# Kernel optimization log

Measured on AMD Instinct MI355X. Metric: run time of the kernel, lower is better.

The kernel has to match this reference:

```python
import jax, jax.numpy as jnp
import numpy as np

N, E = 50000, 800000
D = 64          # output_dim == d_s == d_e
H = 128         # psi hidden width
PSI_IN = 2 * D + 2 * D + D  # 320


def setup_inputs() -> dict:
    key = jax.random.key(0)
    ks = jax.random.split(key, 12)
    scale = lambda fan_in: 1.0 / np.sqrt(fan_in)
    return {
        "h_d_prev": jax.random.normal(ks[0], (N, D), jnp.float32),
        "h_s": jax.random.normal(ks[1], (N, D), jnp.float32),
        "edge_feat": jax.random.normal(ks[2], (E, D), jnp.float32),
        "sender": jax.random.randint(ks[3], (E,), 0, N, jnp.int32),
        "receiver": jax.random.randint(ks[4], (E,), 0, N, jnp.int32),
        # psi MLP params (all layers use relu, incl. last: final_activation=None)
        "W0": jax.random.normal(ks[5], (PSI_IN, H), jnp.float32) * scale(PSI_IN),
        "b0": jnp.zeros((H,), jnp.float32),
        "W1": jax.random.normal(ks[6], (H, H), jnp.float32) * scale(H),
        "b1": jnp.zeros((H,), jnp.float32),
        "W2": jax.random.normal(ks[7], (H, D), jnp.float32) * scale(H),
        "b2": jnp.zeros((D,), jnp.float32),
        # final linear transform W (no bias)
        "Wm": jax.random.normal(ks[8], (D, D), jnp.float32) * scale(D),
    }


def reference(h_d_prev, h_s, edge_feat, sender, receiver, W0, b0, W1, b1, W2, b2, Wm):
    # gather node feats to edges
    h_di = h_d_prev[sender]      # [E, D]
    h_dj = h_d_prev[receiver]    # [E, D]
    h_si = h_s[sender]           # [E, D]
    h_sj = h_s[receiver]         # [E, D]
    psi_in = jnp.concatenate([h_si, h_sj, h_di, h_dj, edge_feat], axis=-1)  # [E, 320]
    # psi MLP: relu on every layer (final_activation=None keeps default relu)
    x = jax.nn.relu(psi_in @ W0 + b0)
    x = jax.nn.relu(x @ W1 + b1)
    psi = jax.nn.relu(x @ W2 + b2)          # [E, D]
    s_ij = psi * (h_dj - h_di)              # [E, D]
    agg = jax.ops.segment_sum(s_ij, receiver, num_segments=h_d_prev.shape[0])  # [N, D]
    return h_d_prev + agg @ Wm
```

## Files before the change

### kernel.cpp

```cpp
#include <hip/hip_runtime.h>

#define NN   50000
#define EE   800000
#define DD   64
#define HH   128
#define KIN  320
#define TILE_E 128

typedef __bf16 bf16x8 __attribute__((ext_vector_type(8)));
typedef float  f32x4  __attribute__((ext_vector_type(4)));

#if __has_builtin(__builtin_amdgcn_cvt_pk_bf16_f32)
typedef __bf16 bf16x2_t __attribute__((ext_vector_type(2)));
__device__ __forceinline__ unsigned int pk2(float a, float b) {
  union { bf16x2_t v; unsigned int u; } cv;
  cv.v = __builtin_amdgcn_cvt_pk_bf16_f32(a, b);
  return cv.u;
}
__device__ __forceinline__ unsigned short f2bf(float a) {
  return (unsigned short)(pk2(a, a) & 0xFFFFu);
}
#else
__device__ __forceinline__ unsigned short f2bf(float f) {
  union { float f; unsigned int u; } v; v.f = f;
  unsigned int u = v.u + 0x7FFFu + ((v.u >> 16) & 1u);
  return (unsigned short)(u >> 16);
}
__device__ __forceinline__ unsigned int pk2(float a, float b) {
  return (unsigned int)f2bf(a) | ((unsigned int)f2bf(b) << 16);
}
#endif

__device__ __forceinline__ float bf2f(unsigned short b) {
  union { unsigned int u; float f; } v; v.u = ((unsigned int)b) << 16; return v.f;
}

__device__ __forceinline__ int psiIdx(int row, int kk) {
  return ((((row >> 4) * 10 + (kk >> 5)) << 6) + ((row & 15) << 2) + ((kk >> 3) & 3)) * 8
         + (kk & 7);
}

__global__ __launch_bounds__(256) void prep_all(
    const float* __restrict__ hd, const float* __restrict__ hs,
    const float* __restrict__ W0, const float* __restrict__ W1,
    const float* __restrict__ W2,
    unsigned short* __restrict__ hdb, unsigned short* __restrict__ hsb,
    unsigned short* __restrict__ WT0, unsigned short* __restrict__ WT1,
    unsigned short* __restrict__ WT2, float* __restrict__ agg) {
  int b = blockIdx.x;
  int t = b * 256 + threadIdx.x;
  if (b < 3125) {
    *(float4*)(agg + (size_t)t * 4) = (float4){0.f, 0.f, 0.f, 0.f};
    const int n = NN * DD / 8;
    const float* src; unsigned short* dst; int i;
    if (t < n) { src = hd; dst = hdb; i = t; }
    else       { src = hs; dst = hsb; i = t - n; }
    float4 a = *(const float4*)(src + (size_t)i * 8);
    float4 c = *(const float4*)(src + (size_t)i * 8 + 4);
    uint4 w;
    w.x = pk2(a.x, a.y); w.y = pk2(a.z, a.w);
    w.z = pk2(c.x, c.y); w.w = pk2(c.z, c.w);
    *(uint4*)(dst + (size_t)i * 8) = w;
  } else {
    int u = t - 3125 * 256;
    if (u < KIN * HH) {
      int k = u / HH, n2 = u % HH;
      WT0[n2 * KIN + k] = f2bf(W0[u]);
    } else if (u < KIN * HH + HH * HH) {
      int v = u - KIN * HH; int k = v / HH, n2 = v % HH;
      WT1[n2 * HH + k] = f2bf(W1[v]);
    } else {
      int v = u - KIN * HH - HH * HH; int k = v / DD, n2 = v % DD;
      WT2[n2 * HH + k] = f2bf(W2[v]);
    }
  }
}

__global__ __launch_bounds__(512, 4) void edge_mlp(
    const unsigned short* __restrict__ hdb,
    const unsigned short* __restrict__ hsb,
    const float* __restrict__ ef,
    const int* __restrict__ snd,
    const int* __restrict__ rcv,
    const unsigned short* __restrict__ WT0,
    const float* __restrict__ b0,
    const unsigned short* __restrict__ WT1,
    const float* __restrict__ b1,
    const unsigned short* __restrict__ WT2,
    const float* __restrict__ b2,
    float* __restrict__ agg)
{
  __shared__ __align__(16) unsigned short psi[TILE_E * KIN];

  const int tid  = threadIdx.x;
  const int e0   = blockIdx.x * TILE_E;
  const int wv   = tid >> 6;
  const int lane = tid & 63;
  const int ln   = lane & 15;
  const int quad = lane >> 4;
  const int mtb  = (wv >> 2) * 4;

  int ridx[16];
  #pragma unroll
  for (int mt = 0; mt < 4; ++mt)
    #pragma unroll
    for (int i = 0; i < 4; ++i)
      ridx[mt * 4 + i] = rcv[e0 + (mtb + mt) * 16 + quad * 4 + i];

  {
    const int eA = tid >> 3;
    const int eB = eA + 64;
    const int c  = tid & 7;
    const int siA = snd[e0 + eA], siB = snd[e0 + eB];
    const int riA = rcv[e0 + eA], riB = rcv[e0 + eB];
    uint4 w[10];
    #pragma unroll
    for (int i = 0; i < 10; ++i) {
      const int seg = i >> 1;
      if (seg < 4) {
        const unsigned short* tb = (seg & 2) ? hdb : hsb;
        int ix = (seg & 1) ? ((i & 1) ? riB : riA)
                           : ((i & 1) ? siB : siA);
        w[i] = *(const uint4*)(tb + (size_t)ix * DD + c * 8);
      } else {
        const int e = (i & 1) ? eB : eA;
        const float* src = ef + (size_t)(e0 + e) * DD + c * 8;
        float4 v0 = *(const float4*)(src);
        float4 v1 = *(const float4*)(src + 4);
        w[i].x = pk2(v0.x, v0.y); w[i].y = pk2(v0.z, v0.w);
        w[i].z = pk2(v1.x, v1.y); w[i].w = pk2(v1.z, v1.w);
      }
    }
    #pragma unroll
    for (int i = 0; i < 10; ++i) {
      const int seg = i >> 1;
      const int e   = (i & 1) ? eB : eA;
      int unit = (((e >> 4) * 10 + seg * 2 + (c >> 2)) << 6) + ((e & 15) << 2) + (c & 3);
      *(uint4*)(&psi[unit * 8]) = w[i];
    }
  }

  const int col = wv * 16 + ln;

  bf16x8 wf[10];
  {
    const unsigned short* wb = WT0 + col * KIN + quad * 8;
    #pragma unroll
    for (int k0 = 0; k0 < 10; ++k0) wf[k0] = *(const bf16x8*)(wb + k0 * 32);
  }
  __syncthreads();

  f32x4 acc[8];

  #pragma unroll
  for (int m = 0; m < 8; ++m) acc[m] = (f32x4){0,0,0,0};
  #pragma unroll
  for (int k0 = 0; k0 < 10; ++k0)
    #pragma unroll
    for (int mt = 0; mt < 8; ++mt) {
      bf16x8 af = *(const bf16x8*)(&psi[(((mt * 10 + k0) << 6) + (ln << 2) + quad) * 8]);
      acc[mt] = __builtin_amdgcn_mfma_f32_16x16x32_bf16(af, wf[k0], acc[mt], 0, 0, 0);
    }
  __syncthreads();

  {
    float bv = b0[col];
    #pragma unroll
    for (int mt = 0; mt < 8; ++mt)
      #pragma unroll
      for (int i = 0; i < 4; ++i) {
        int row = mt * 16 + quad * 4 + i;
        float v = acc[mt][i] + bv; v = v > 0.f ? v : 0.f;
        psi[psiIdx(row, col)] = f2bf(v);
      }
  }
  bf16x8 wg[4];
  {
    const unsigned short* wb = WT1 + col * HH + quad * 8;
    #pragma unroll
    for (int k0 = 0; k0 < 4; ++k0) wg[k0] = *(const bf16x8*)(wb + k0 * 32);
  }
  __syncthreads();

  #pragma unroll
  for (int m = 0; m < 8; ++m) acc[m] = (f32x4){0,0,0,0};
  #pragma unroll
  for (int k0 = 0; k0 < 4; ++k0)
    #pragma unroll
    for (int mt = 0; mt < 8; ++mt) {
      bf16x8 af = *(const bf16x8*)(&psi[(((mt * 10 + k0) << 6) + (ln << 2) + quad) * 8]);
      acc[mt] = __builtin_amdgcn_mfma_f32_16x16x32_bf16(af, wg[k0], acc[mt], 0, 0, 0);
    }
  __syncthreads();

  {
    float bv = b1[col];
    #pragma unroll
    for (int mt = 0; mt < 8; ++mt)
      #pragma unroll
      for (int i = 0; i < 4; ++i) {
        int row = mt * 16 + quad * 4 + i;
        float v = acc[mt][i] + bv; v = v > 0.f ? v : 0.f;
        psi[psiIdx(row, col)] = f2bf(v);
      }
  }
  const int col2 = (wv & 3) * 16 + ln;
  bf16x8 wh[4];
  {
    const unsigned short* wb = WT2 + col2 * HH + quad * 8;
    #pragma unroll
    for (int k0 = 0; k0 < 4; ++k0) wh[k0] = *(const bf16x8*)(wb + k0 * 32);
  }
  __syncthreads();

  {
    f32x4 acc2[4];
    #pragma unroll
    for (int m = 0; m < 4; ++m) acc2[m] = (f32x4){0,0,0,0};
    #pragma unroll
    for (int k0 = 0; k0 < 4; ++k0)
      #pragma unroll
      for (int m = 0; m < 4; ++m) {
        int mt = mtb + m;
        bf16x8 af = *(const bf16x8*)(&psi[(((mt * 10 + k0) << 6) + (ln << 2) + quad) * 8]);
        acc2[m] = __builtin_amdgcn_mfma_f32_16x16x32_bf16(af, wh[k0], acc2[m], 0, 0, 0);
      }
    float bv = b2[col2];
    #pragma unroll
    for (int m = 0; m < 4; ++m)
      #pragma unroll
      for (int i = 0; i < 4; ++i) {
        int row = (mtb + m) * 16 + quad * 4 + i;
        float p  = acc2[m][i] + bv; p = p > 0.f ? p : 0.f;
        float di = bf2f(psi[psiIdx(row, 128 + col2)]);
        float dj = bf2f(psi[psiIdx(row, 192 + col2)]);
        float s  = p * (dj - di);
        atomicAdd(&agg[(size_t)ridx[m * 4 + i] * DD + col2], s);
      }
  }
}

__global__ __launch_bounds__(256) void final_out(
    const float* __restrict__ hd,
    const float* __restrict__ agg,
    const float* __restrict__ Wm,
    float* __restrict__ out)
{
  __shared__ float wmf[DD * DD];
  __shared__ float arow[16 * 72];
  int tid = threadIdx.x;
  const float4* wm4 = (const float4*)Wm;
  float4* wf4 = (float4*)wmf;
  #pragma unroll
  for (int i = tid; i < DD * DD / 4; i += 256) wf4[i] = wm4[i];

  int r0 = blockIdx.x * 16;
  {
    float4 av = *(const float4*)(agg + (size_t)r0 * DD + tid * 4);
    int rr = tid >> 4, cc = (tid & 15) * 4;
    *(float4*)&arow[rr * 72 + cc] = av;
  }
  __syncthreads();

  int row = tid >> 4;
  int cq  = (tid & 15) * 4;
  f32x4 acc = (f32x4){0, 0, 0, 0};
  #pragma unroll
  for (int k = 0; k < DD; ++k) {
    float a = arow[row * 72 + k];
    f32x4 w = *(const f32x4*)&wmf[k * DD + cq];
    acc += a * w;
  }
  size_t o = ((size_t)(r0 + row)) * DD + cq;
  f32x4 h = *(const f32x4*)(hd + o);
  *(f32x4*)(out + o) = h + acc;
}

extern "C" void kernel_launch(void* const* d_in, const int* in_sizes, int n_in,
                              void* d_out, int out_size, void* d_ws, size_t ws_size,
                              hipStream_t stream) {
  const float* hd = (const float*)d_in[0];
  const float* hs = (const float*)d_in[1];
  const float* ef = (const float*)d_in[2];
  const int* snd  = (const int*)d_in[3];
  const int* rcv  = (const int*)d_in[4];
  const float* W0 = (const float*)d_in[5];
  const float* b0 = (const float*)d_in[6];
  const float* W1 = (const float*)d_in[7];
  const float* b1 = (const float*)d_in[8];
  const float* W2 = (const float*)d_in[9];
  const float* b2 = (const float*)d_in[10];
  const float* Wm = (const float*)d_in[11];
  float* out      = (float*)d_out;

  char* ws = (char*)d_ws;
  float* agg = (float*)ws;
  unsigned short* WT0 = (unsigned short*)(ws + 12800000);
  unsigned short* WT1 = WT0 + KIN * HH;
  unsigned short* WT2 = WT1 + HH * HH;
  unsigned short* hdb = WT2 + HH * DD;
  unsigned short* hsb = hdb + (size_t)NN * DD;
  prep_all<<<3381, 256, 0, stream>>>(hd, hs, W0, W1, W2,
                                     hdb, hsb, WT0, WT1, WT2, agg);
  edge_mlp<<<EE / TILE_E, 512, 0, stream>>>(hdb, hsb, ef, snd, rcv,
                                            WT0, b0, WT1, b1, WT2, b2, agg);
  final_out<<<NN / 16, 256, 0, stream>>>(hd, agg, Wm, out);
}
```

Baseline: 521.0 us.

## Switch edge MLP to 32x32x16 MFMA tiles with XOR-swizzled LDS layout

```diff
diff --git a/kernel.cpp b/kernel.cpp
--- a/kernel.cpp
+++ b/kernel.cpp
@@ -9,6 +9,7 @@
 
 typedef __bf16 bf16x8 __attribute__((ext_vector_type(8)));
 typedef float  f32x4  __attribute__((ext_vector_type(4)));
+typedef float  f32x16 __attribute__((ext_vector_type(16)));
 
 #if __has_builtin(__builtin_amdgcn_cvt_pk_bf16_f32)
 typedef __bf16 bf16x2_t __attribute__((ext_vector_type(2)));
@@ -36,8 +37,9 @@
 }
 
 __device__ __forceinline__ int psiIdx(int row, int kk) {
-  return ((((row >> 4) * 10 + (kk >> 5)) << 6) + ((row & 15) << 2) + ((kk >> 3) & 3)) * 8
-         + (kk & 7);
+  int u = (((row >> 4) * 10 + (kk >> 5)) << 6) + ((row & 15) << 2) + ((kk >> 3) & 3);
+  u ^= (row >> 1) & 3;
+  return (u << 3) + (kk & 7);
 }
 
 __global__ __launch_bounds__(256) void prep_all(
@@ -96,21 +98,25 @@
   const int e0   = blockIdx.x * TILE_E;
   const int wv   = tid >> 6;
   const int lane = tid & 63;
-  const int ln   = lane & 15;
-  const int quad = lane >> 4;
-  const int mtb  = (wv >> 2) * 4;
-
-  int ridx[16];
-  #pragma unroll
-  for (int mt = 0; mt < 4; ++mt)
-    #pragma unroll
-    for (int i = 0; i < 4; ++i)
-      ridx[mt * 4 + i] = rcv[e0 + (mtb + mt) * 16 + quad * 4 + i];
+  const int l31  = lane & 31;
+  const int g2   = lane >> 5;
+
+  const int et = wv & 3;
+  const int hp = (wv >> 2) << 1;
+  const int nt = wv >> 2;
+
+  int rv[16];
+  #pragma unroll
+  for (int reg = 0; reg < 16; ++reg) {
+    int row = et * 32 + (reg & 3) + ((reg >> 2) << 3) + (g2 << 2);
+    rv[reg] = rcv[e0 + row];
+  }
 
   {
     const int eA = tid >> 3;
     const int eB = eA + 64;
     const int c  = tid & 7;
+    const int sw = (eA >> 1) & 3;
     const int siA = snd[e0 + eA], siB = snd[e0 + eB];
     const int riA = rcv[e0 + eA], riB = rcv[e0 + eB];
     uint4 w[10];
@@ -136,107 +142,100 @@
       const int seg = i >> 1;
       const int e   = (i & 1) ? eB : eA;
       int unit = (((e >> 4) * 10 + seg * 2 + (c >> 2)) << 6) + ((e & 15) << 2) + (c & 3);
+      unit ^= sw;
       *(uint4*)(&psi[unit * 8]) = w[i];
     }
   }
 
-  const int col = wv * 16 + ln;
-
-  bf16x8 wf[10];
-  {
-    const unsigned short* wb = WT0 + col * KIN + quad * 8;
-    #pragma unroll
-    for (int k0 = 0; k0 < 10; ++k0) wf[k0] = *(const bf16x8*)(wb + k0 * 32);
-  }
-  __syncthreads();
-
-  f32x4 acc[8];
-
-  #pragma unroll
-  for (int m = 0; m < 8; ++m) acc[m] = (f32x4){0,0,0,0};
-  #pragma unroll
-  for (int k0 = 0; k0 < 10; ++k0)
-    #pragma unroll
-    for (int mt = 0; mt < 8; ++mt) {
-      bf16x8 af = *(const bf16x8*)(&psi[(((mt * 10 + k0) << 6) + (ln << 2) + quad) * 8]);
-      acc[mt] = __builtin_amdgcn_mfma_f32_16x16x32_bf16(af, wf[k0], acc[mt], 0, 0, 0);
-    }
-  __syncthreads();
-
-  {
-    float bv = b0[col];
-    #pragma unroll
-    for (int mt = 0; mt < 8; ++mt)
-      #pragma unroll
-      for (int i = 0; i < 4; ++i) {
-        int row = mt * 16 + quad * 4 + i;
-        float v = acc[mt][i] + bv; v = v > 0.f ? v : 0.f;
-        psi[psiIdx(row, col)] = f2bf(v);
-      }
-  }
-  bf16x8 wg[4];
-  {
-    const unsigned short* wb = WT1 + col * HH + quad * 8;
-    #pragma unroll
-    for (int k0 = 0; k0 < 4; ++k0) wg[k0] = *(const bf16x8*)(wb + k0 * 32);
-  }
-  __syncthreads();
-
-  #pragma unroll
-  for (int m = 0; m < 8; ++m) acc[m] = (f32x4){0,0,0,0};
-  #pragma unroll
-  for (int k0 = 0; k0 < 4; ++k0)
-    #pragma unroll
-    for (int mt = 0; mt < 8; ++mt) {
-      bf16x8 af = *(const bf16x8*)(&psi[(((mt * 10 + k0) << 6) + (ln << 2) + quad) * 8]);
-      acc[mt] = __builtin_amdgcn_mfma_f32_16x16x32_bf16(af, wg[k0], acc[mt], 0, 0, 0);
-    }
-  __syncthreads();
-
-  {
-    float bv = b1[col];
-    #pragma unroll
-    for (int mt = 0; mt < 8; ++mt)
-      #pragma unroll
-      for (int i = 0; i < 4; ++i) {
-        int row = mt * 16 + quad * 4 + i;
-        float v = acc[mt][i] + bv; v = v > 0.f ? v : 0.f;
-        psi[psiIdx(row, col)] = f2bf(v);
-      }
-  }
-  const int col2 = (wv & 3) * 16 + ln;
-  bf16x8 wh[4];
-  {
-    const unsigned short* wb = WT2 + col2 * HH + quad * 8;
-    #pragma unroll
-    for (int k0 = 0; k0 < 4; ++k0) wh[k0] = *(const bf16x8*)(wb + k0 * 32);
-  }
-  __syncthreads();
-
-  {
-    f32x4 acc2[4];
-    #pragma unroll
-    for (int m = 0; m < 4; ++m) acc2[m] = (f32x4){0,0,0,0};
-    #pragma unroll
-    for (int k0 = 0; k0 < 4; ++k0)
-      #pragma unroll
-      for (int m = 0; m < 4; ++m) {
-        int mt = mtb + m;
-        bf16x8 af = *(const bf16x8*)(&psi[(((mt * 10 + k0) << 6) + (ln << 2) + quad) * 8]);
-        acc2[m] = __builtin_amdgcn_mfma_f32_16x16x32_bf16(af, wh[k0], acc2[m], 0, 0, 0);
-      }
-    float bv = b2[col2];
-    #pragma unroll
-    for (int m = 0; m < 4; ++m)
-      #pragma unroll
-      for (int i = 0; i < 4; ++i) {
-        int row = (mtb + m) * 16 + quad * 4 + i;
-        float p  = acc2[m][i] + bv; p = p > 0.f ? p : 0.f;
-        float di = bf2f(psi[psiIdx(row, 128 + col2)]);
-        float dj = bf2f(psi[psiIdx(row, 192 + col2)]);
-        float s  = p * (dj - di);
-        atomicAdd(&agg[(size_t)ridx[m * 4 + i] * DD + col2], s);
-      }
+  const int arow = et * 32 + l31;
+
+  const unsigned short* wb0 = WT0 + (hp * 32 + l31) * KIN + g2 * 8;
+  const unsigned short* wb1 = wb0 + 32 * KIN;
+  bf16x8 p0[2], p1[2];
+  #pragma unroll
+  for (int k0 = 0; k0 < 2; ++k0) {
+    p0[k0] = *(const bf16x8*)(wb0 + k0 * 16);
+    p1[k0] = *(const bf16x8*)(wb1 + k0 * 16);
+  }
+  __syncthreads();
+
+  f32x16 acc0 = {0,0,0,0,0,0,0,0,0,0,0,0,0,0,0,0};
+  f32x16 acc1 = {0,0,0,0,0,0,0,0,0,0,0,0,0,0,0,0};
+
+  #pragma unroll
+  for (int k0 = 0; k0 < 20; ++k0) {
+    bf16x8 a   = *(const bf16x8*)(&psi[psiIdx(arow, k0 * 16 + g2 * 8)]);
+    bf16x8 bf0 = (k0 < 2) ? p0[k0] : *(const bf16x8*)(wb0 + k0 * 16);
+    bf16x8 bf1 = (k0 < 2) ? p1[k0] : *(const bf16x8*)(wb1 + k0 * 16);
+    acc0 = __builtin_amdgcn_mfma_f32_32x32x16_bf16(a, bf0, acc0, 0, 0, 0);
+    acc1 = __builtin_amdgcn_mfma_f32_32x32x16_bf16(a, bf1, acc1, 0, 0, 0);
+  }
+  __syncthreads();
+
+  {
+    const int col0 = hp * 32 + l31, col1 = col0 + 32;
+    float bv0 = b0[col0], bv1 = b0[col1];
+    #pragma unroll
+    for (int reg = 0; reg < 16; ++reg) {
+      int row = et * 32 + (reg & 3) + ((reg >> 2) << 3) + (g2 << 2);
+      float v0 = acc0[reg] + bv0; v0 = v0 > 0.f ? v0 : 0.f;
+      float v1 = acc1[reg] + bv1; v1 = v1 > 0.f ? v1 : 0.f;
+      psi[psiIdx(row, col0)] = f2bf(v0);
+      psi[psiIdx(row, col1)] = f2bf(v1);
+    }
+  }
+  __syncthreads();
+
+  acc0 = (f32x16){0,0,0,0,0,0,0,0,0,0,0,0,0,0,0,0};
+  acc1 = (f32x16){0,0,0,0,0,0,0,0,0,0,0,0,0,0,0,0};
+  {
+    const unsigned short* wc0 = WT1 + (hp * 32 + l31) * HH + g2 * 8;
+    const unsigned short* wc1 = wc0 + 32 * HH;
+    #pragma unroll
+    for (int k0 = 0; k0 < 8; ++k0) {
+      bf16x8 a   = *(const bf16x8*)(&psi[psiIdx(arow, k0 * 16 + g2 * 8)]);
+      bf16x8 bf0 = *(const bf16x8*)(wc0 + k0 * 16);
+      bf16x8 bf1 = *(const bf16x8*)(wc1 + k0 * 16);
+      acc0 = __builtin_amdgcn_mfma_f32_32x32x16_bf16(a, bf0, acc0, 0, 0, 0);
+      acc1 = __builtin_amdgcn_mfma_f32_32x32x16_bf16(a, bf1, acc1, 0, 0, 0);
+    }
+  }
+  __syncthreads();
+
+  {
+    const int col0 = hp * 32 + l31, col1 = col0 + 32;
+    float bv0 = b1[col0], bv1 = b1[col1];
+    #pragma unroll
+    for (int reg = 0; reg < 16; ++reg) {
+      int row = et * 32 + (reg & 3) + ((reg >> 2) << 3) + (g2 << 2);
+      float v0 = acc0[reg] + bv0; v0 = v0 > 0.f ? v0 : 0.f;
+      float v1 = acc1[reg] + bv1; v1 = v1 > 0.f ? v1 : 0.f;
+      psi[psiIdx(row, col0)] = f2bf(v0);
+      psi[psiIdx(row, col1)] = f2bf(v1);
+    }
+  }
+  __syncthreads();
+
+  {
+    f32x16 acc2 = {0,0,0,0,0,0,0,0,0,0,0,0,0,0,0,0};
+    const unsigned short* wd = WT2 + (nt * 32 + l31) * HH + g2 * 8;
+    #pragma unroll
+    for (int k0 = 0; k0 < 8; ++k0) {
+      bf16x8 a  = *(const bf16x8*)(&psi[psiIdx(arow, k0 * 16 + g2 * 8)]);
+      bf16x8 bf = *(const bf16x8*)(wd + k0 * 16);
+      acc2 = __builtin_amdgcn_mfma_f32_32x32x16_bf16(a, bf, acc2, 0, 0, 0);
+    }
+    int   n2 = nt * 32 + l31;
+    float bv = b2[n2];
+    #pragma unroll
+    for (int reg = 0; reg < 16; ++reg) {
+      int row = et * 32 + (reg & 3) + ((reg >> 2) << 3) + (g2 << 2);
+      float p  = acc2[reg] + bv; p = p > 0.f ? p : 0.f;
+      float di = bf2f(psi[psiIdx(row, 128 + n2)]);
+      float dj = bf2f(psi[psiIdx(row, 192 + n2)]);
+      float s  = p * (dj - di);
+      atomicAdd(&agg[(size_t)rv[reg] * DD + n2], s);
+    }
   }
 }
 
```

Measured after the change: 786.4 us. 50.9% more time.

## Precompute per-node first-layer projections and gather them instead of raw features

Applied to the files above, without the earlier changes.

```diff
diff --git a/kernel.cpp b/kernel.cpp
--- a/kernel.cpp
+++ b/kernel.cpp
@@ -31,37 +31,45 @@
 }
 #endif
 
-__device__ __forceinline__ float bf2f(unsigned short b) {
-  union { unsigned int u; float f; } v; v.u = ((unsigned int)b) << 16; return v.f;
+__device__ __forceinline__ float bitsf(unsigned int u) {
+  union { unsigned int u; float f; } v; v.u = u; return v.f;
+}
+__device__ __forceinline__ void ub2(unsigned int u, float& lo, float& hi) {
+  lo = bitsf(u << 16); hi = bitsf(u & 0xFFFF0000u);
+}
+__device__ __forceinline__ unsigned int addbf2(unsigned int a, unsigned int r) {
+  float a0, a1, r0, r1; ub2(a, a0, a1); ub2(r, r0, r1);
+  return pk2(a0 + r0, a1 + r1);
 }
 
 __device__ __forceinline__ int psiIdx(int row, int kk) {
-  return ((((row >> 4) * 10 + (kk >> 5)) << 6) + ((row & 15) << 2) + ((kk >> 3) & 3)) * 8
-         + (kk & 7);
+  int u = (((row >> 4) * 10 + (kk >> 5)) << 6) + ((row & 15) << 2) + ((kk >> 3) & 3);
+  u ^= (row >> 1) & 3;
+  return (u << 3) + (kk & 7);
 }
 
 __global__ __launch_bounds__(256) void prep_all(
     const float* __restrict__ hd, const float* __restrict__ hs,
-    const float* __restrict__ W0, const float* __restrict__ W1,
-    const float* __restrict__ W2,
-    unsigned short* __restrict__ hdb, unsigned short* __restrict__ hsb,
+    const float* __restrict__ W0, const float* __restrict__ b0,
+    const float* __restrict__ W1, const float* __restrict__ W2,
+    unsigned short* __restrict__ hdb,
     unsigned short* __restrict__ WT0, unsigned short* __restrict__ WT1,
-    unsigned short* __restrict__ WT2, float* __restrict__ agg) {
+    unsigned short* __restrict__ WT2,
+    unsigned short* __restrict__ As, unsigned short* __restrict__ Ar,
+    float* __restrict__ agg) {
   int b = blockIdx.x;
   int t = b * 256 + threadIdx.x;
   if (b < 3125) {
     *(float4*)(agg + (size_t)t * 4) = (float4){0.f, 0.f, 0.f, 0.f};
-    const int n = NN * DD / 8;
-    const float* src; unsigned short* dst; int i;
-    if (t < n) { src = hd; dst = hdb; i = t; }
-    else       { src = hs; dst = hsb; i = t - n; }
-    float4 a = *(const float4*)(src + (size_t)i * 8);
-    float4 c = *(const float4*)(src + (size_t)i * 8 + 4);
-    uint4 w;
-    w.x = pk2(a.x, a.y); w.y = pk2(a.z, a.w);
-    w.z = pk2(c.x, c.y); w.w = pk2(c.z, c.w);
-    *(uint4*)(dst + (size_t)i * 8) = w;
-  } else {
+    if (t < NN * DD / 8) {
+      float4 a = *(const float4*)(hd + (size_t)t * 8);
+      float4 c = *(const float4*)(hd + (size_t)t * 8 + 4);
+      uint4 w;
+      w.x = pk2(a.x, a.y); w.y = pk2(a.z, a.w);
+      w.z = pk2(c.x, c.y); w.w = pk2(c.z, c.w);
+      *(uint4*)(hdb + (size_t)t * 8) = w;
+    }
+  } else if (b < 3381) {
     int u = t - 3125 * 256;
     if (u < KIN * HH) {
       int k = u / HH, n2 = u % HH;
@@ -73,17 +81,92 @@
       int v = u - KIN * HH - HH * HH; int k = v / DD, n2 = v % DD;
       WT2[n2 * HH + k] = f2bf(W2[v]);
     }
+  } else {
+    int pb = b - 3381;
+    int nb = pb * 64;
+    int w  = threadIdx.x >> 6;
+    int l  = threadIdx.x & 63, ln = l & 15, quad = l >> 4;
+
+    bf16x8 af[4][4];
+    float4 b0v[4];
+    #pragma unroll
+    for (int ct = 0; ct < 4; ++ct) {
+      int ctg  = w * 4 + ct;
+      int colt = ((ctg & 7) << 4) + ln;
+      int roff = (ctg >= 8) ? 64 : 0;
+      #pragma unroll
+      for (int k0 = 0; k0 < 4; ++k0) {
+        int kb   = k0 * 32 + quad * 8;
+        int wrow = ((kb < 64) ? kb : kb + 64) + roff;
+        union { unsigned int u[4]; bf16x8 v; } cv;
+        #pragma unroll
+        for (int j = 0; j < 4; ++j) {
+          float fa = W0[(size_t)(wrow + 2 * j) * HH + colt];
+          float fb = W0[(size_t)(wrow + 2 * j + 1) * HH + colt];
+          cv.u[j] = pk2(fa, fb);
+        }
+        af[ct][k0] = cv.v;
+      }
+      if (ctg < 8) b0v[ct] = *(const float4*)&b0[((ctg & 7) << 4) + (quad << 2)];
+      else         b0v[ct] = (float4){0.f, 0.f, 0.f, 0.f};
+    }
+
+    f32x4 acc[4][4];
+    #pragma unroll
+    for (int ct = 0; ct < 4; ++ct)
+      #pragma unroll
+      for (int nt = 0; nt < 4; ++nt) acc[ct][nt] = (f32x4){0, 0, 0, 0};
+
+    #pragma unroll
+    for (int nt = 0; nt < 4; ++nt) {
+      int node = nb + nt * 16 + ln;
+      if (node > NN - 1) node = NN - 1;
+      #pragma unroll
+      for (int k0 = 0; k0 < 4; ++k0) {
+        int kb = k0 * 32 + quad * 8;
+        const float* src = (kb < 64) ? (hs + (size_t)node * DD + kb)
+                                     : (hd + (size_t)node * DD + (kb - 64));
+        float4 v0 = *(const float4*)src;
+        float4 v1 = *(const float4*)(src + 4);
+        union { unsigned int u[4]; bf16x8 v; } cv;
+        cv.u[0] = pk2(v0.x, v0.y); cv.u[1] = pk2(v0.z, v0.w);
+        cv.u[2] = pk2(v1.x, v1.y); cv.u[3] = pk2(v1.z, v1.w);
+        #pragma unroll
+        for (int ct = 0; ct < 4; ++ct)
+          acc[ct][nt] = __builtin_amdgcn_mfma_f32_16x16x32_bf16(
+              af[ct][k0], cv.v, acc[ct][nt], 0, 0, 0);
+      }
+    }
+
+    #pragma unroll
+    for (int ct = 0; ct < 4; ++ct) {
+      int ctg = w * 4 + ct;
+      unsigned short* T = (ctg < 8) ? As : Ar;
+      int cb = ((ctg & 7) << 4) + (quad << 2);
+      #pragma unroll
+      for (int nt = 0; nt < 4; ++nt) {
+        int node = nb + nt * 16 + ln;
+        if (node < NN) {
+          float v0 = acc[ct][nt][0] + b0v[ct].x;
+          float v1 = acc[ct][nt][1] + b0v[ct].y;
+          float v2 = acc[ct][nt][2] + b0v[ct].z;
+          float v3 = acc[ct][nt][3] + b0v[ct].w;
+          uint2 o; o.x = pk2(v0, v1); o.y = pk2(v2, v3);
+          *(uint2*)(T + (size_t)node * HH + cb) = o;
+        }
+      }
+    }
   }
 }
 
 __global__ __launch_bounds__(512, 4) void edge_mlp(
+    const unsigned short* __restrict__ As,
+    const unsigned short* __restrict__ Ar,
     const unsigned short* __restrict__ hdb,
-    const unsigned short* __restrict__ hsb,
     const float* __restrict__ ef,
     const int* __restrict__ snd,
     const int* __restrict__ rcv,
     const unsigned short* __restrict__ WT0,
-    const float* __restrict__ b0,
     const unsigned short* __restrict__ WT1,
     const float* __restrict__ b1,
     const unsigned short* __restrict__ WT2,
@@ -95,148 +178,183 @@
   const int tid  = threadIdx.x;
   const int e0   = blockIdx.x * TILE_E;
   const int wv   = tid >> 6;
-  const int lane = tid & 63;
-  const int ln   = lane & 15;
-  const int quad = lane >> 4;
-  const int mtb  = (wv >> 2) * 4;
-
-  int ridx[16];
-  #pragma unroll
-  for (int mt = 0; mt < 4; ++mt)
-    #pragma unroll
-    for (int i = 0; i < 4; ++i)
-      ridx[mt * 4 + i] = rcv[e0 + (mtb + mt) * 16 + quad * 4 + i];
+  const int ln   = tid & 15;
+  const int quad = (tid >> 4) & 3;
+  const int hctp = wv >> 1;
+  const int ebL  = (wv & 1) * 4;
+  const int w2ct = wv & 3;
+  const int ebE  = (wv >> 2) * 4;
+
+  int rv[4];
+  #pragma unroll
+  for (int et = 0; et < 4; ++et) rv[et] = rcv[e0 + (ebE + et) * 16 + ln];
 
   {
-    const int eA = tid >> 3;
-    const int eB = eA + 64;
-    const int c  = tid & 7;
-    const int siA = snd[e0 + eA], siB = snd[e0 + eB];
-    const int riA = rcv[e0 + eA], riB = rcv[e0 + eB];
-    uint4 w[10];
-    #pragma unroll
-    for (int i = 0; i < 10; ++i) {
-      const int seg = i >> 1;
-      if (seg < 4) {
-        const unsigned short* tb = (seg & 2) ? hdb : hsb;
-        int ix = (seg & 1) ? ((i & 1) ? riB : riA)
-                           : ((i & 1) ? siB : siA);
-        w[i] = *(const uint4*)(tb + (size_t)ix * DD + c * 8);
+    uint4 st[5]; int ua[5];
+    #pragma unroll
+    for (int k = 0; k < 5; ++k) {
+      if (k < 4) {
+        int j = tid + k * 512;
+        int e = j >> 4, c = j & 15;
+        int si = snd[e0 + e], ri = rcv[e0 + e];
+        uint4 a = *(const uint4*)(As + (size_t)si * HH + c * 8);
+        uint4 r = *(const uint4*)(Ar + (size_t)ri * HH + c * 8);
+        st[k].x = addbf2(a.x, r.x); st[k].y = addbf2(a.y, r.y);
+        st[k].z = addbf2(a.z, r.z); st[k].w = addbf2(a.w, r.w);
+        ua[k] = psiIdx(e, c * 8);
       } else {
-        const int e = (i & 1) ? eB : eA;
-        const float* src = ef + (size_t)(e0 + e) * DD + c * 8;
-        float4 v0 = *(const float4*)(src);
-        float4 v1 = *(const float4*)(src + 4);
-        w[i].x = pk2(v0.x, v0.y); w[i].y = pk2(v0.z, v0.w);
-        w[i].z = pk2(v1.x, v1.y); w[i].w = pk2(v1.z, v1.w);
+        int e = tid >> 3, c = tid & 7;
+        st[k] = *(const uint4*)(hdb + (size_t)snd[e0 + e] * DD + c * 8);
+        ua[k] = psiIdx(e, 128 + c * 8);
       }
     }
     #pragma unroll
-    for (int i = 0; i < 10; ++i) {
-      const int seg = i >> 1;
-      const int e   = (i & 1) ? eB : eA;
-      int unit = (((e >> 4) * 10 + seg * 2 + (c >> 2)) << 6) + ((e & 15) << 2) + (c & 3);
-      *(uint4*)(&psi[unit * 8]) = w[i];
-    }
+    for (int k = 0; k < 5; ++k) *(uint4*)&psi[ua[k]] = st[k];
+    #pragma unroll
+    for (int k = 5; k < 10; ++k) {
+      uint4 v; int u;
+      if (k == 5) {
+        int e = 64 + (tid >> 3), c = tid & 7;
+        v = *(const uint4*)(hdb + (size_t)snd[e0 + e] * DD + c * 8);
+        u = psiIdx(e, 128 + c * 8);
+      } else if (k < 8) {
+        int idx = tid + (k - 6) * 512;
+        int e = idx >> 3, c = idx & 7;
+        v = *(const uint4*)(hdb + (size_t)rcv[e0 + e] * DD + c * 8);
+        u = psiIdx(e, 192 + c * 8);
+      } else {
+        int idx = tid + (k - 8) * 512;
+        int e = idx >> 3, c = idx & 7;
+        const float* s = ef + (size_t)(e0 + e) * DD + c * 8;
+        float4 v0 = *(const float4*)s, v1 = *(const float4*)(s + 4);
+        v.x = pk2(v0.x, v0.y); v.y = pk2(v0.z, v0.w);
+        v.z = pk2(v1.x, v1.y); v.w = pk2(v1.z, v1.w);
+        u = psiIdx(e, 256 + c * 8);
+      }
+      st[k - 5] = v; ua[k - 5] = u;
+    }
+    #pragma unroll
+    for (int k = 0; k < 5; ++k) *(uint4*)&psi[ua[k]] = st[k];
   }
 
-  const int col = wv * 16 + ln;
-
-  bf16x8 wf[10];
-  {
-    const unsigned short* wb = WT0 + col * KIN + quad * 8;
-    #pragma unroll
-    for (int k0 = 0; k0 < 10; ++k0) wf[k0] = *(const bf16x8*)(wb + k0 * 32);
-  }
+  bf16x8 wa[2][2];
+  #pragma unroll
+  for (int hh = 0; hh < 2; ++hh)
+    #pragma unroll
+    for (int k2 = 0; k2 < 2; ++k2)
+      wa[hh][k2] = *(const bf16x8*)(WT0
+          + (size_t)((hctp * 2 + hh) * 16 + ln) * KIN + 256 + k2 * 32 + quad * 8);
   __syncthreads();
 
-  f32x4 acc[8];
-
-  #pragma unroll
-  for (int m = 0; m < 8; ++m) acc[m] = (f32x4){0,0,0,0};
-  #pragma unroll
-  for (int k0 = 0; k0 < 10; ++k0)
-    #pragma unroll
-    for (int mt = 0; mt < 8; ++mt) {
-      bf16x8 af = *(const bf16x8*)(&psi[(((mt * 10 + k0) << 6) + (ln << 2) + quad) * 8]);
-      acc[mt] = __builtin_amdgcn_mfma_f32_16x16x32_bf16(af, wf[k0], acc[mt], 0, 0, 0);
-    }
+  f32x4 acc[2][4];
+  #pragma unroll
+  for (int hh = 0; hh < 2; ++hh)
+    #pragma unroll
+    for (int et = 0; et < 4; ++et) acc[hh][et] = (f32x4){0, 0, 0, 0};
+
+  #pragma unroll
+  for (int k2 = 0; k2 < 2; ++k2)
+    #pragma unroll
+    for (int et = 0; et < 4; ++et) {
+      bf16x8 bfr = *(const bf16x8*)&psi[psiIdx((ebL + et) * 16 + ln,
+                                               256 + k2 * 32 + quad * 8)];
+      acc[0][et] = __builtin_amdgcn_mfma_f32_16x16x32_bf16(wa[0][k2], bfr, acc[0][et], 0, 0, 0);
+      acc[1][et] = __builtin_amdgcn_mfma_f32_16x16x32_bf16(wa[1][k2], bfr, acc[1][et], 0, 0, 0);
+    }
+
+  #pragma unroll
+  for (int hh = 0; hh < 2; ++hh)
+    #pragma unroll
+    for (int et = 0; et < 4; ++et) {
+      int e  = (ebL + et) * 16 + ln;
+      int bi = psiIdx(e, (hctp * 2 + hh) * 16 + quad * 4);
+      uint2 aw = *(uint2*)&psi[bi];
+      float f0, f1, f2, f3; ub2(aw.x, f0, f1); ub2(aw.y, f2, f3);
+      float v0 = fmaxf(acc[hh][et][0] + f0, 0.f);
+      float v1 = fmaxf(acc[hh][et][1] + f1, 0.f);
+      float v2 = fmaxf(acc[hh][et][2] + f2, 0.f);
+      float v3 = fmaxf(acc[hh][et][3] + f3, 0.f);
+      uint2 o; o.x = pk2(v0, v1); o.y = pk2(v2, v3);
+      *(uint2*)&psi[bi] = o;
+    }
+
+  bf16x8 wb[2][4];
+  #pragma unroll
+  for (int hh = 0; hh < 2; ++hh)
+    #pragma unroll
+    for (int k0 = 0; k0 < 4; ++k0)
+      wb[hh][k0] = *(const bf16x8*)(WT1
+          + (size_t)((hctp * 2 + hh) * 16 + ln) * HH + k0 * 32 + quad * 8);
+  float4 b1v[2];
+  #pragma unroll
+  for (int hh = 0; hh < 2; ++hh)
+    b1v[hh] = *(const float4*)&b1[(hctp * 2 + hh) * 16 + quad * 4];
   __syncthreads();
 
-  {
-    float bv = b0[col];
-    #pragma unroll
-    for (int mt = 0; mt < 8; ++mt)
-      #pragma unroll
-      for (int i = 0; i < 4; ++i) {
-        int row = mt * 16 + quad * 4 + i;
-        float v = acc[mt][i] + bv; v = v > 0.f ? v : 0.f;
-        psi[psiIdx(row, col)] = f2bf(v);
-      }
-  }
-  bf16x8 wg[4];
-  {
-    const unsigned short* wb = WT1 + col * HH + quad * 8;
-    #pragma unroll
-    for (int k0 = 0; k0 < 4; ++k0) wg[k0] = *(const bf16x8*)(wb + k0 * 32);
-  }
+  #pragma unroll
+  for (int hh = 0; hh < 2; ++hh)
+    #pragma unroll
+    for (int et = 0; et < 4; ++et) acc[hh][et] = (f32x4){0, 0, 0, 0};
+  #pragma unroll
+  for (int k0 = 0; k0 < 4; ++k0)
+    #pragma unroll
+    for (int et = 0; et < 4; ++et) {
+      bf16x8 bfr = *(const bf16x8*)&psi[psiIdx((ebL + et) * 16 + ln,
+                                               k0 * 32 + quad * 8)];
+      acc[0][et] = __builtin_amdgcn_mfma_f32_16x16x32_bf16(wb[0][k0], bfr, acc[0][et], 0, 0, 0);
+      acc[1][et] = __builtin_amdgcn_mfma_f32_16x16x32_bf16(wb[1][k0], bfr, acc[1][et], 0, 0, 0);
+    }
+
+  bf16x8 wc[4];
+  #pragma unroll
+  for (int k0 = 0; k0 < 4; ++k0)
+    wc[k0] = *(const bf16x8*)(WT2 + (size_t)(w2ct * 16 + ln) * HH + k0 * 32 + quad * 8);
+  float4 b2v = *(const float4*)&b2[w2ct * 16 + quad * 4];
   __syncthreads();
 
   #pragma unroll
-  for (int m = 0; m < 8; ++m) acc[m] = (f32x4){0,0,0,0};
+  for (int hh = 0; hh < 2; ++hh)
+    #pragma unroll
+    for (int et = 0; et < 4; ++et) {
+      int e  = (ebL + et) * 16 + ln;
+      int bi = psiIdx(e, (hctp * 2 + hh) * 16 + quad * 4);
+      float v0 = fmaxf(acc[hh][et][0] + b1v[hh].x, 0.f);
+      float v1 = fmaxf(acc[hh][et][1] + b1v[hh].y, 0.f);
+      float v2 = fmaxf(acc[hh][et][2] + b1v[hh].z, 0.f);
+      float v3 = fmaxf(acc[hh][et][3] + b1v[hh].w, 0.f);
+      uint2 o; o.x = pk2(v0, v1); o.y = pk2(v2, v3);
+      *(uint2*)&psi[bi] = o;
+    }
+  __syncthreads();
+
+  f32x4 a2[4];
+  #pragma unroll
+  for (int et = 0; et < 4; ++et) a2[et] = (f32x4){0, 0, 0, 0};
   #pragma unroll
   for (int k0 = 0; k0 < 4; ++k0)
     #pragma unroll
-    for (int mt = 0; mt < 8; ++mt) {
-      bf16x8 af = *(const bf16x8*)(&psi[(((mt * 10 + k0) << 6) + (ln << 2) + quad) * 8]);
-      acc[mt] = __builtin_amdgcn_mfma_f32_16x16x32_bf16(af, wg[k0], acc[mt], 0, 0, 0);
-    }
-  __syncthreads();
-
-  {
-    float bv = b1[col];
-    #pragma unroll
-    for (int mt = 0; mt < 8; ++mt)
-      #pragma unroll
-      for (int i = 0; i < 4; ++i) {
-        int row = mt * 16 + quad * 4 + i;
-        float v = acc[mt][i] + bv; v = v > 0.f ? v : 0.f;
-        psi[psiIdx(row, col)] = f2bf(v);
-      }
-  }
-  const int col2 = (wv & 3) * 16 + ln;
-  bf16x8 wh[4];
-  {
-    const unsigned short* wb = WT2 + col2 * HH + quad * 8;
-    #pragma unroll
-    for (int k0 = 0; k0 < 4; ++k0) wh[k0] = *(const bf16x8*)(wb + k0 * 32);
-  }
-  __syncthreads();
-
-  {
-    f32x4 acc2[4];
-    #pragma unroll
-    for (int m = 0; m < 4; ++m) acc2[m] = (f32x4){0,0,0,0};
-    #pragma unroll
-    for (int k0 = 0; k0 < 4; ++k0)
-      #pragma unroll
-      for (int m = 0; m < 4; ++m) {
-        int mt = mtb + m;
-        bf16x8 af = *(const bf16x8*)(&psi[(((mt * 10 + k0) << 6) + (ln << 2) + quad) * 8]);
-        acc2[m] = __builtin_amdgcn_mfma_f32_16x16x32_bf16(af, wh[k0], acc2[m], 0, 0, 0);
-      }
-    float bv = b2[col2];
-    #pragma unroll
-    for (int m = 0; m < 4; ++m)
-      #pragma unroll
-      for (int i = 0; i < 4; ++i) {
-        int row = (mtb + m) * 16 + quad * 4 + i;
-        float p  = acc2[m][i] + bv; p = p > 0.f ? p : 0.f;
-        float di = bf2f(psi[psiIdx(row, 128 + col2)]);
-        float dj = bf2f(psi[psiIdx(row, 192 + col2)]);
-        float s  = p * (dj - di);
-        atomicAdd(&agg[(size_t)ridx[m * 4 + i] * DD + col2], s);
-      }
+    for (int et = 0; et < 4; ++et) {
+      bf16x8 bfr = *(const bf16x8*)&psi[psiIdx((ebE + et) * 16 + ln,
+                                               k0 * 32 + quad * 8)];
+      a2[et] = __builtin_amdgcn_mfma_f32_16x16x32_bf16(wc[k0], bfr, a2[et], 0, 0, 0);
+    }
+  #pragma unroll
+  for (int et = 0; et < 4; ++et) {
+    int e = (ebE + et) * 16 + ln;
+    uint2 du = *(uint2*)&psi[psiIdx(e, 128 + w2ct * 16 + quad * 4)];
+    uint2 dv = *(uint2*)&psi[psiIdx(e, 192 + w2ct * 16 + quad * 4)];
+    float di0, di1, di2, di3, dj0, dj1, dj2, dj3;
+    ub2(du.x, di0, di1); ub2(du.y, di2, di3);
+    ub2(dv.x, dj0, dj1); ub2(dv.y, dj2, dj3);
+    float p0 = fmaxf(a2[et][0] + b2v.x, 0.f);
+    float p1 = fmaxf(a2[et][1] + b2v.y, 0.f);
+    float p2 = fmaxf(a2[et][2] + b2v.z, 0.f);
+    float p3 = fmaxf(a2[et][3] + b2v.w, 0.f);
+    size_t base = (size_t)rv[et] * DD + w2ct * 16 + quad * 4;
+    atomicAdd(&agg[base + 0], p0 * (dj0 - di0));
+    atomicAdd(&agg[base + 1], p1 * (dj1 - di1));
+    atomicAdd(&agg[base + 2], p2 * (dj2 - di2));
+    atomicAdd(&agg[base + 3], p3 * (dj3 - di3));
   }
 }
 
@@ -298,11 +416,12 @@
   unsigned short* WT0 = (unsigned short*)(ws + 12800000);
   unsigned short* WT1 = WT0 + KIN * HH;
   unsigned short* WT2 = WT1 + HH * HH;
-  unsigned short* hdb = WT2 + HH * DD;
-  unsigned short* hsb = hdb + (size_t)NN * DD;
-  prep_all<<<3381, 256, 0, stream>>>(hd, hs, W0, W1, W2,
-                                     hdb, hsb, WT0, WT1, WT2, agg);
-  edge_mlp<<<EE / TILE_E, 512, 0, stream>>>(hdb, hsb, ef, snd, rcv,
-                                            WT0, b0, WT1, b1, WT2, b2, agg);
+  unsigned short* hdb = (unsigned short*)(ws + 12931072);
+  unsigned short* As  = (unsigned short*)(ws + 19331072);
+  unsigned short* Ar  = (unsigned short*)(ws + 32131072);
+  prep_all<<<4163, 256, 0, stream>>>(hd, hs, W0, b0, W1, W2,
+                                     hdb, WT0, WT1, WT2, As, Ar, agg);
+  edge_mlp<<<EE / TILE_E, 512, 0, stream>>>(As, Ar, hdb, ef, snd, rcv,
+                                            WT0, WT1, b1, WT2, b2, agg);
   final_out<<<NN / 16, 256, 0, stream>>>(hd, agg, Wm, out);
 }
```

After: 1.002 ms. 92.4% more time.
